# Optimization experiments

Hardware: AMD Instinct MI355X
Metric: run time of the kernel (lower is better)

The kernel has to match this reference:

```python
import jax, jax.numpy as jnp
import numpy as np

N_PRIMES = 50
BATCH = 4096
DIM = 8192
GOLDEN_RATIO = (1.0 + np.sqrt(5.0)) / 2.0


def _generate_primes(n):
    primes = []
    num = 2
    while len(primes) < n:
        if all(num % p != 0 for p in primes):
            primes.append(num)
        num += 1
    return np.array(primes, dtype=np.int32)


def setup_inputs() -> dict:
    key = jax.random.key(0)
    k1, k2, k3 = jax.random.split(key, 3)
    return {
        "token_hash": jax.random.randint(k3, (BATCH,), 0, 1000000000, dtype=jnp.int32),
        "primes": jnp.asarray(_generate_primes(N_PRIMES)),  # [50] int32, constant
        "resonance_scales": jax.random.normal(k1, (N_PRIMES,), dtype=jnp.float32),
        "phase_shifts": jax.random.normal(k2, (N_PRIMES,), dtype=jnp.float32),
        "energy_preservation": jnp.asarray(1.0, dtype=jnp.float32),
        "dimension": DIM,
    }


def reference(token_hash, primes, resonance_scales, phase_shifts, energy_preservation, dimension):
    n_primes = primes.shape[0]
    idx = jnp.arange(dimension) % n_primes                      # [D] prime index per spectrum slot
    p = primes[idx].astype(jnp.float32)                         # [D]
    base_freq = p * (GOLDEN_RATIO * np.pi / dimension)          # [D]
    scale = jax.nn.sigmoid(resonance_scales[idx])               # [D]
    freq = base_freq * scale * energy_preservation              # [D]
    # token modulation: (token_hash % 1000) / 1000
    tm = (token_hash % 1000).astype(jnp.float32) / 1000.0       # [B]
    angle = phase_shifts[idx][None, :] + tm[:, None] * (2.0 * np.pi)  # [B, D]
    spectrum = freq[None, :] * (1.0 + 0.1 * jnp.sin(angle))     # [B, D]
    norm = jnp.linalg.norm(spectrum, axis=-1, keepdims=True)    # [B, 1]
    spectrum = jnp.where(norm > 0, spectrum * energy_preservation / norm, spectrum)
    return spectrum
```

## Files before the change

kernel.cpp:

```cpp
#include <hip/hip_runtime.h>
#include <math.h>


#define PHI_PI  5.083203692315259f
#define TWO_PI  6.2831853071795864769f

__global__ __launch_bounds__(256) void phrs_kernel(
    const int*   __restrict__ token_hash,
    const int*   __restrict__ primes,
    const float* __restrict__ rscales,
    const float* __restrict__ pshifts,
    const float* __restrict__ energy,
    float*       __restrict__ out,
    int B, int D, int NP)
{
    const int w    = threadIdx.x >> 6;
    const int lane = threadIdx.x & 63;
    const int b    = blockIdx.x * 4 + w;
    if (b >= B) return;

    const float E = energy[0];

    float s = 0.0f;
    if (lane < NP) {
        const float tm    = (float)(token_hash[b] % 1000) * 1e-3f;
        const float p     = (float)primes[lane];
        const float sig   = 1.0f / (1.0f + expf(-rscales[lane]));
        const float freq  = p * (PHI_PI / (float)D) * sig * E;
        const float angle = pshifts[lane] + tm * TWO_PI;
        s = freq * (1.0f + 0.1f * sinf(angle));
    }

    const int q = D / NP, r = D % NP;
    float red = (lane < NP) ? (float)(q + (lane < r ? 1 : 0)) * s * s : 0.0f;
    #pragma unroll
    for (int off = 32; off; off >>= 1)
        red += __shfl_xor(red, off, 64);
    const float inv = (red > 0.0f) ? (E / sqrtf(red)) : 1.0f;

    if (NP == 50 && (D & 3) == 0) {
        int i0 = (4 * lane) % 50;
        int i1 = i0 + 1; if (i1 >= 50) i1 -= 50;
        int i2 = i0 + 2; if (i2 >= 50) i2 -= 50;
        int i3 = i0 + 3; if (i3 >= 50) i3 -= 50;
        float4 v;
        v.x = __shfl(s, i0, 64) * inv;
        v.y = __shfl(s, i1, 64) * inv;
        v.z = __shfl(s, i2, 64) * inv;
        v.w = __shfl(s, i3, 64) * inv;

        if (lane < 50) {
            float4* __restrict__ out4 = reinterpret_cast<float4*>(out);
            const int nv = D >> 2;
            const size_t base = (size_t)b * (size_t)nv;
            #pragma unroll 8
            for (int o = lane; o < nv; o += 50)
                out4[base + o] = v;
        }
    } else {
        const size_t rowbase = (size_t)b * (size_t)D;
        for (int i = lane; i < D; i += 64) {
            float sv = __shfl(s, i % NP, 64);
            out[rowbase + i] = sv * inv;
        }
    }
}

extern "C" void kernel_launch(void* const* d_in, const int* in_sizes, int n_in,
                              void* d_out, int out_size, void* d_ws, size_t ws_size,
                              hipStream_t stream) {
    const int*   token_hash = (const int*)  d_in[0];
    const int*   primes     = (const int*)  d_in[1];
    const float* rscales    = (const float*)d_in[2];
    const float* pshifts    = (const float*)d_in[3];
    const float* energy     = (const float*)d_in[4];
    float*       out        = (float*)      d_out;

    const int B  = in_sizes[0];
    const int NP = in_sizes[1];
    const int D  = out_size / B;

    const int blocks = (B + 3) / 4;
    phrs_kernel<<<dim3(blocks), dim3(256), 0, stream>>>(
        token_hash, primes, rscales, pshifts, energy, out, B, D, NP);
}
```

Measured before the change: 28.14 us.

## Store rows with full 64-lane nontemporal writes using an LDS pattern

The 25-entry float4 repeating pattern (two periods of the 50 primes) is staged in shared memory per wave. All 64 lanes then store with a rotating index instead of only 50 lanes, so each wavefront store covers a contiguous 1 KB span. The stores are nontemporal, and the fast __expf/__sinf intrinsics are used. The aim is higher write bandwidth on this store-bound kernel. The cost is slightly lower transcendental precision and a stricter D%256 condition for the fast path.

```diff
diff --git a/kernel.cpp b/kernel.cpp
--- a/kernel.cpp
+++ b/kernel.cpp
@@ -4,6 +4,8 @@
 
 #define PHI_PI  5.083203692315259f
 #define TWO_PI  6.2831853071795864769f
+
+typedef float f32x4 __attribute__((ext_vector_type(4)));
 
 __global__ __launch_bounds__(256) void phrs_kernel(
     const int*   __restrict__ token_hash,
@@ -14,6 +16,8 @@
     float*       __restrict__ out,
     int B, int D, int NP)
 {
+    __shared__ f32x4 s_pat[4][32];
+
     const int w    = threadIdx.x >> 6;
     const int lane = threadIdx.x & 63;
     const int b    = blockIdx.x * 4 + w;
@@ -21,15 +25,13 @@
 
     const float E = energy[0];
 
-    float s = 0.0f;
-    if (lane < NP) {
-        const float tm    = (float)(token_hash[b] % 1000) * 1e-3f;
-        const float p     = (float)primes[lane];
-        const float sig   = 1.0f / (1.0f + expf(-rscales[lane]));
-        const float freq  = p * (PHI_PI / (float)D) * sig * E;
-        const float angle = pshifts[lane] + tm * TWO_PI;
-        s = freq * (1.0f + 0.1f * sinf(angle));
-    }
+    const int jc      = (lane < NP) ? lane : (NP - 1);
+    const float tm    = (float)(token_hash[b] % 1000) * 1e-3f;
+    const float p     = (float)primes[jc];
+    const float sig   = 1.0f / (1.0f + __expf(-rscales[jc]));
+    const float freq  = p * (PHI_PI / (float)D) * sig * E;
+    const float angle = pshifts[jc] + tm * TWO_PI;
+    const float s     = freq * (1.0f + 0.1f * __sinf(angle));
 
     const int q = D / NP, r = D % NP;
     float red = (lane < NP) ? (float)(q + (lane < r ? 1 : 0)) * s * s : 0.0f;
@@ -38,24 +40,30 @@
         red += __shfl_xor(red, off, 64);
     const float inv = (red > 0.0f) ? (E / sqrtf(red)) : 1.0f;
 
-    if (NP == 50 && (D & 3) == 0) {
+    if (NP == 50 && (D & 255) == 0) {
         int i0 = (4 * lane) % 50;
         int i1 = i0 + 1; if (i1 >= 50) i1 -= 50;
         int i2 = i0 + 2; if (i2 >= 50) i2 -= 50;
         int i3 = i0 + 3; if (i3 >= 50) i3 -= 50;
-        float4 v;
+        f32x4 v;
         v.x = __shfl(s, i0, 64) * inv;
         v.y = __shfl(s, i1, 64) * inv;
         v.z = __shfl(s, i2, 64) * inv;
         v.w = __shfl(s, i3, 64) * inv;
+        if (lane < 25) s_pat[w][lane] = v;
 
-        if (lane < 50) {
-            float4* __restrict__ out4 = reinterpret_cast<float4*>(out);
-            const int nv = D >> 2;
-            const size_t base = (size_t)b * (size_t)nv;
-            #pragma unroll 8
-            for (int o = lane; o < nv; o += 50)
-                out4[base + o] = v;
+        f32x4* __restrict__ out4 = reinterpret_cast<f32x4*>(out);
+        const int nv = D >> 2;
+        const size_t base = (size_t)b * (size_t)nv;
+        int rmod = lane;
+        if (rmod >= 25) rmod -= 25;
+        if (rmod >= 25) rmod -= 25;
+        #pragma unroll 8
+        for (int k = lane; k < nv; k += 64) {
+            f32x4 pv = s_pat[w][rmod];
+            __builtin_nontemporal_store(pv, &out4[base + k]);
+            rmod += 14;
+            if (rmod >= 25) rmod -= 25;
         }
     } else {
         const size_t rowbase = (size_t)b * (size_t)D;
```

Result: faster. 27.16 us (-3.5%).
